# Performance work log

Hardware: AMD Instinct MI355X
Metric: run time of the kernel (lower is better)

Reference implementation:

```python
import jax, jax.numpy as jnp
import numpy as np

K_NEIGHBOURS = 40  # includes self; self is dropped after top-k


def setup_inputs() -> dict:
    key = jax.random.key(0)
    ks = jax.random.split(key, 4)
    B, V, F_in = 4, 4096, 64
    P, S, F_out = 64, 4, 64
    x = jax.random.normal(ks[0], (B, V, F_in), dtype=jnp.float32)
    Wf = jax.random.normal(ks[1], (F_in, P), dtype=jnp.float32) / np.sqrt(F_in)
    bf = jnp.zeros((P,), dtype=jnp.float32)
    Ws = jax.random.normal(ks[2], (F_in, S), dtype=jnp.float32) / np.sqrt(F_in)
    bs = jnp.zeros((S,), dtype=jnp.float32)
    Wo = jax.random.normal(ks[3], (F_in + 2 * P, F_out), dtype=jnp.float32) / np.sqrt(F_in + 2 * P)
    bo = jnpp = jnp.zeros((F_out,), dtype=jnp.float32)
    return {"x": x, "Wf": Wf, "bf": bf, "Ws": Ws, "bs": bs, "Wo": Wo, "bo": bo}


def _euclidean_squared(c):
    # c: [B, V, S] -> [B, V, V] squared pairwise distances
    sq = jnp.sum(c * c, axis=-1)  # [B, V]
    d2 = sq[:, :, None] + sq[:, None, :] - 2.0 * jnp.einsum('bvs,bus->bvu', c, c)
    return d2


def reference(x, Wf, bf, Ws, bs, Wo, bo):
    # learned spatial coordinates and propagated features
    coords = x @ Ws + bs            # [B, V, S]
    feats = x @ Wf + bf             # [B, V, P]

    d2 = _euclidean_squared(coords)                 # [B, V, V]
    neg_vals, idx = jax.lax.top_k(-d2, K_NEIGHBOURS)  # closest first (self at 0)
    nbr_idx = idx[:, :, 1:]                         # [B, V, K-1]
    dist = -neg_vals[:, :, 1:]                      # [B, V, K-1] (>= 0)

    # gauss_of_lin(d * 10) = exp(-|10 d|)
    w = jnp.exp(-jnp.abs(dist * 10.0))              # [B, V, K-1]

    # gather neighbour features per batch: [B, V, K-1, P]
    nf = jax.vmap(lambda f, i: f[i])(feats, nbr_idx)
    nf = nf * w[..., None]

    collected = jnp.concatenate([jnp.max(nf, axis=2), jnp.mean(nf, axis=2)], axis=-1)  # [B, V, 2P]
    updated = jnp.concatenate([x, collected], axis=-1)  # [B, V, F_in + 2P]
    return jnp.tanh(updated @ Wo + bo)
```

## Files before the change

kernel.cpp:

```cpp
#include <hip/hip_runtime.h>
#include <cmath>

#define BB  4
#define VV  4096
#define KK  40
#define FIN 64

typedef float v2f __attribute__((ext_vector_type(2)));

__global__ __launch_bounds__(256) void prep_kernel(
    const float* __restrict__ x, const float* __restrict__ Wf,
    const float* __restrict__ bf, const float* __restrict__ Ws,
    const float* __restrict__ bs,
    float* __restrict__ coords, float* __restrict__ sq,
    float* __restrict__ feats)
{
    int lane = threadIdx.x & 63;
    int wid  = threadIdx.x >> 6;
    int row0 = (blockIdx.x * 4 + wid) * 4;
    const float* xr = x + (size_t)row0 * FIN;

    float a0 = 0.f, a1 = 0.f, a2 = 0.f, a3 = 0.f;
    #pragma unroll 8
    for (int k = 0; k < FIN; ++k) {
        float wf = Wf[k * 64 + lane];
        a0 = fmaf(xr[k],        wf, a0);
        a1 = fmaf(xr[64  + k],  wf, a1);
        a2 = fmaf(xr[128 + k],  wf, a2);
        a3 = fmaf(xr[192 + k],  wf, a3);
    }
    float bfl = bf[lane];
    feats[(size_t)(row0 + 0) * 64 + lane] = a0 + bfl;
    feats[(size_t)(row0 + 1) * 64 + lane] = a1 + bfl;
    feats[(size_t)(row0 + 2) * 64 + lane] = a2 + bfl;
    feats[(size_t)(row0 + 3) * 64 + lane] = a3 + bfl;

    int r  = lane >> 4;
    int s  = (lane >> 2) & 3;
    int kc = lane & 3;
    const float* xrr = x + (size_t)(row0 + r) * FIN + kc * 16;
    const float* wsr = Ws + kc * 16 * 4 + s;
    float c = 0.f;
    #pragma unroll
    for (int k = 0; k < 16; ++k)
        c = fmaf(xrr[k], wsr[k * 4], c);
    c += __shfl_xor(c, 1, 64);
    c += __shfl_xor(c, 2, 64);
    float val = c + bs[s];
    if ((lane & 3) == 0) coords[(size_t)(row0 + r) * 4 + s] = val;
    float p = val * val;
    p += __shfl_xor(p, 4, 64);
    p += __shfl_xor(p, 8, 64);
    if ((lane & 15) == 0) sq[row0 + r] = p;
}

__device__ __forceinline__ unsigned umed3(unsigned a, unsigned b, unsigned c)
{
    unsigned d;
    asm("v_med3_u32 %0, %1, %2, %3" : "=v"(d) : "v"(a), "v"(b), "v"(c));
    return d;
}

__device__ __forceinline__ int cnt_lt4(unsigned m0, unsigned m1,
                                       unsigned m2, unsigned m3,
                                       unsigned cand)
{
    return (int)__popcll(__ballot(m0 < cand))
         + (int)__popcll(__ballot(m1 < cand))
         + (int)__popcll(__ballot(m2 < cand))
         + (int)__popcll(__ballot(m3 < cand));
}

__device__ __forceinline__ unsigned select_thresh(unsigned m0, unsigned m1,
                                                  unsigned m2, unsigned m3)
{
    unsigned M = 0u;
    #pragma unroll
    for (int bit = 30; bit >= 12; --bit) {
        unsigned cand = M | (1u << bit);
        if (cnt_lt4(m0, m1, m2, m3, cand) <= 39) M = cand;
    }
    unsigned Msel = M | 0xFFFu;
    if (cnt_lt4(m0, m1, m2, m3, M + 4096u) != 40) {
        #pragma unroll
        for (int bit = 11; bit >= 0; --bit) {
            unsigned cand = M | (1u << bit);
            if (cnt_lt4(m0, m1, m2, m3, cand) <= 39) M = cand;
        }
        Msel = M;
    }
    return Msel;
}

__device__ __forceinline__ void compact4(unsigned m0, unsigned m1,
                                         unsigned m2, unsigned m3,
                                         unsigned Msel, uint2* dst)
{
    unsigned mn = m0;
    #pragma unroll
    for (int off = 32; off >= 1; off >>= 1) {
        unsigned o = __shfl_xor(mn, off, 64);
        mn = o < mn ? o : mn;
    }
    int base = 0;
    unsigned kk = m0;
    #pragma unroll
    for (int i = 0; i < 4; ++i) {
        bool pred = (kk <= Msel) && (kk != mn);
        unsigned long long mask = __ballot(pred);
        unsigned pos = (unsigned)base +
            __builtin_amdgcn_mbcnt_hi((unsigned)(mask >> 32),
                __builtin_amdgcn_mbcnt_lo((unsigned)mask, 0u));
        if (pred) {
            float d2a = __uint_as_float(kk & 0xFFFFF000u);
            float w   = __expf(-10.f * d2a);
            dst[pos] = make_uint2((kk & 4095u) << 8, __float_as_uint(w));
        }
        base += (int)__popcll(mask);
        kk = (i == 0) ? m1 : (i == 1) ? m2 : m3;
    }
}

__global__ __launch_bounds__(256) void gravnet_kernel(
    const float* __restrict__ x, const float* __restrict__ coords,
    const float* __restrict__ sq, const float* __restrict__ feats,
    const float* __restrict__ Wo, const float* __restrict__ bo,
    float* __restrict__ out)
{
    int lane = threadIdx.x & 63;
    int wid  = threadIdx.x >> 6;
    int q0   = (blockIdx.x * 4 + wid) * 4;
    int b    = q0 >> 12;
    int v0   = q0 & (VV - 1);

    __shared__ uint2               s_nb[4][4][KK];
    __shared__ __align__(16) float s_upd[4][4][192];

    const float4* cb  = (const float4*)(coords + (size_t)b * VV * 4);
    const float*  sqb = sq + (size_t)b * VV;

    float4 cq0 = cb[v0],     cq1 = cb[v0 + 1];
    float4 cq2 = cb[v0 + 2], cq3 = cb[v0 + 3];
    v2f nxA = (v2f){-2.f * cq0.x, -2.f * cq1.x};
    v2f nyA = (v2f){-2.f * cq0.y, -2.f * cq1.y};
    v2f nzA = (v2f){-2.f * cq0.z, -2.f * cq1.z};
    v2f nwA = (v2f){-2.f * cq0.w, -2.f * cq1.w};
    v2f hsA = (v2f){sqb[v0], sqb[v0 + 1]};
    v2f nxB = (v2f){-2.f * cq2.x, -2.f * cq3.x};
    v2f nyB = (v2f){-2.f * cq2.y, -2.f * cq3.y};
    v2f nzB = (v2f){-2.f * cq2.z, -2.f * cq3.z};
    v2f nwB = (v2f){-2.f * cq2.w, -2.f * cq3.w};
    v2f hsB = (v2f){sqb[v0 + 2], sqb[v0 + 3]};

    unsigned k00 = ~0u, k01 = ~0u, k02 = ~0u, k03 = ~0u;
    unsigned k10 = ~0u, k11 = ~0u, k12 = ~0u, k13 = ~0u;
    unsigned k20 = ~0u, k21 = ~0u, k22 = ~0u, k23 = ~0u;
    unsigned k30 = ~0u, k31 = ~0u, k32 = ~0u, k33 = ~0u;

    #pragma unroll 4
    for (int i = 0; i < 64; ++i) {
        int u = i * 64 + lane;
        float4 cu = cb[u];
        float squ = sqb[u];
        v2f accA = hsA + (v2f){squ, squ};
        accA = __builtin_elementwise_fma(nxA, (v2f){cu.x, cu.x}, accA);
        accA = __builtin_elementwise_fma(nyA, (v2f){cu.y, cu.y}, accA);
        accA = __builtin_elementwise_fma(nzA, (v2f){cu.z, cu.z}, accA);
        accA = __builtin_elementwise_fma(nwA, (v2f){cu.w, cu.w}, accA);
        v2f accB = hsB + (v2f){squ, squ};
        accB = __builtin_elementwise_fma(nxB, (v2f){cu.x, cu.x}, accB);
        accB = __builtin_elementwise_fma(nyB, (v2f){cu.y, cu.y}, accB);
        accB = __builtin_elementwise_fma(nzB, (v2f){cu.z, cu.z}, accB);
        accB = __builtin_elementwise_fma(nwB, (v2f){cu.w, cu.w}, accB);

        {
            float d2 = fmaxf(accA.x, 0.f);
            unsigned k = (__float_as_uint(d2) & 0xFFFFF000u) | (unsigned)u;
            unsigned n1 = umed3(k00, k01, k);
            unsigned n2 = umed3(k01, k02, k);
            unsigned n3 = umed3(k02, k03, k);
            k00 = min(k00, k); k01 = n1; k02 = n2; k03 = n3;
        }
        {
            float d2 = fmaxf(accA.y, 0.f);
            unsigned k = (__float_as_uint(d2) & 0xFFFFF000u) | (unsigned)u;
            unsigned n1 = umed3(k10, k11, k);
            unsigned n2 = umed3(k11, k12, k);
            unsigned n3 = umed3(k12, k13, k);
            k10 = min(k10, k); k11 = n1; k12 = n2; k13 = n3;
        }
        {
            float d2 = fmaxf(accB.x, 0.f);
            unsigned k = (__float_as_uint(d2) & 0xFFFFF000u) | (unsigned)u;
            unsigned n1 = umed3(k20, k21, k);
            unsigned n2 = umed3(k21, k22, k);
            unsigned n3 = umed3(k22, k23, k);
            k20 = min(k20, k); k21 = n1; k22 = n2; k23 = n3;
        }
        {
            float d2 = fmaxf(accB.y, 0.f);
            unsigned k = (__float_as_uint(d2) & 0xFFFFF000u) | (unsigned)u;
            unsigned n1 = umed3(k30, k31, k);
            unsigned n2 = umed3(k31, k32, k);
            unsigned n3 = umed3(k32, k33, k);
            k30 = min(k30, k); k31 = n1; k32 = n2; k33 = n3;
        }
    }

    compact4(k00, k01, k02, k03, select_thresh(k00, k01, k02, k03),
             &s_nb[wid][0][0]);
    compact4(k10, k11, k12, k13, select_thresh(k10, k11, k12, k13),
             &s_nb[wid][1][0]);
    compact4(k20, k21, k22, k23, select_thresh(k20, k21, k22, k23),
             &s_nb[wid][2][0]);
    compact4(k30, k31, k32, k33, select_thresh(k30, k31, k32, k33),
             &s_nb[wid][3][0]);

    const float* fb  = feats + (size_t)b * VV * 64;
    const char*  fbl = (const char*)(fb + lane);
    float vmax0 = -INFINITY, vsum0 = 0.f, vmax1 = -INFINITY, vsum1 = 0.f;
    float vmax2 = -INFINITY, vsum2 = 0.f, vmax3 = -INFINITY, vsum3 = 0.f;
    #pragma unroll 3
    for (int j = 0; j < KK - 1; ++j) {
        uint2 n0 = s_nb[wid][0][j];
        uint2 n1 = s_nb[wid][1][j];
        uint2 n2 = s_nb[wid][2][j];
        uint2 n3 = s_nb[wid][3][j];
        float f0 = *(const float*)(fbl + n0.x);
        float f1 = *(const float*)(fbl + n1.x);
        float f2 = *(const float*)(fbl + n2.x);
        float f3 = *(const float*)(fbl + n3.x);
        float v0g = __uint_as_float(n0.y) * f0;
        float v1g = __uint_as_float(n1.y) * f1;
        float v2g = __uint_as_float(n2.y) * f2;
        float v3g = __uint_as_float(n3.y) * f3;
        vmax0 = fmaxf(vmax0, v0g); vsum0 += v0g;
        vmax1 = fmaxf(vmax1, v1g); vsum1 += v1g;
        vmax2 = fmaxf(vmax2, v2g); vsum2 += v2g;
        vmax3 = fmaxf(vmax3, v3g); vsum3 += v3g;
    }

    s_upd[wid][0][lane]       = x[(size_t)(q0 + 0) * 64 + lane];
    s_upd[wid][0][64  + lane] = vmax0;
    s_upd[wid][0][128 + lane] = vsum0 * (1.0f / 39.0f);
    s_upd[wid][1][lane]       = x[(size_t)(q0 + 1) * 64 + lane];
    s_upd[wid][1][64  + lane] = vmax1;
    s_upd[wid][1][128 + lane] = vsum1 * (1.0f / 39.0f);
    s_upd[wid][2][lane]       = x[(size_t)(q0 + 2) * 64 + lane];
    s_upd[wid][2][64  + lane] = vmax2;
    s_upd[wid][2][128 + lane] = vsum2 * (1.0f / 39.0f);
    s_upd[wid][3][lane]       = x[(size_t)(q0 + 3) * 64 + lane];
    s_upd[wid][3][64  + lane] = vmax3;
    s_upd[wid][3][128 + lane] = vsum3 * (1.0f / 39.0f);

    float bol = bo[lane];
    float acc0 = bol, acc1 = bol, acc2 = bol, acc3 = bol;
    #pragma unroll 4
    for (int j4 = 0; j4 < 48; ++j4) {
        float wo0 = Wo[(j4 * 4 + 0) * 64 + lane];
        float wo1 = Wo[(j4 * 4 + 1) * 64 + lane];
        float wo2 = Wo[(j4 * 4 + 2) * 64 + lane];
        float wo3 = Wo[(j4 * 4 + 3) * 64 + lane];
        float4 u0 = *(const float4*)&s_upd[wid][0][j4 * 4];
        float4 u1 = *(const float4*)&s_upd[wid][1][j4 * 4];
        float4 u2 = *(const float4*)&s_upd[wid][2][j4 * 4];
        float4 u3 = *(const float4*)&s_upd[wid][3][j4 * 4];
        acc0 = fmaf(u0.x, wo0, acc0);  acc1 = fmaf(u1.x, wo0, acc1);
        acc2 = fmaf(u2.x, wo0, acc2);  acc3 = fmaf(u3.x, wo0, acc3);
        acc0 = fmaf(u0.y, wo1, acc0);  acc1 = fmaf(u1.y, wo1, acc1);
        acc2 = fmaf(u2.y, wo1, acc2);  acc3 = fmaf(u3.y, wo1, acc3);
        acc0 = fmaf(u0.z, wo2, acc0);  acc1 = fmaf(u1.z, wo2, acc1);
        acc2 = fmaf(u2.z, wo2, acc2);  acc3 = fmaf(u3.z, wo2, acc3);
        acc0 = fmaf(u0.w, wo3, acc0);  acc1 = fmaf(u1.w, wo3, acc1);
        acc2 = fmaf(u2.w, wo3, acc2);  acc3 = fmaf(u3.w, wo3, acc3);
    }
    float e0 = __expf(2.f * acc0);
    float e1 = __expf(2.f * acc1);
    float e2 = __expf(2.f * acc2);
    float e3 = __expf(2.f * acc3);
    out[(size_t)(q0 + 0) * 64 + lane] = 1.f - __fdividef(2.f, e0 + 1.f);
    out[(size_t)(q0 + 1) * 64 + lane] = 1.f - __fdividef(2.f, e1 + 1.f);
    out[(size_t)(q0 + 2) * 64 + lane] = 1.f - __fdividef(2.f, e2 + 1.f);
    out[(size_t)(q0 + 3) * 64 + lane] = 1.f - __fdividef(2.f, e3 + 1.f);
}

extern "C" void kernel_launch(void* const* d_in, const int* in_sizes, int n_in,
                              void* d_out, int out_size, void* d_ws, size_t ws_size,
                              hipStream_t stream)
{
    (void)in_sizes; (void)n_in; (void)out_size; (void)ws_size;
    const float* x  = (const float*)d_in[0];
    const float* Wf = (const float*)d_in[1];
    const float* bf = (const float*)d_in[2];
    const float* Ws = (const float*)d_in[3];
    const float* bs = (const float*)d_in[4];
    const float* Wo = (const float*)d_in[5];
    const float* bo = (const float*)d_in[6];
    float* out = (float*)d_out;

    float* coords = (float*)d_ws;
    float* sq     = coords + (size_t)BB * VV * 4;
    float* feats  = sq + (size_t)BB * VV;

    prep_kernel<<<BB * VV / 16, 256, 0, stream>>>(x, Wf, bf, Ws, bs,
                                                  coords, sq, feats);
    gravnet_kernel<<<BB * VV / 16, 256, 0, stream>>>(x, coords, sq, feats,
                                                     Wo, bo, out);
}
```

Before: 127.0 us.

## Split candidate scan across wave pairs and merge per-lane top-4 via LDS

Each query group of 4 is now handled by two waves, each scanning half of the candidate points. The per-lane sorted top-4 lists are exchanged through shared memory and merged with a bitonic-style min step, then each wave compacts, gathers and projects 2 of the 4 queries. This doubles the grid and halves the serial scan per wave to increase parallelism, at the cost of block-wide barriers, LDS traffic and duplicated Wo loads.

```diff
diff --git a/kernel.cpp b/kernel.cpp
--- a/kernel.cpp
+++ b/kernel.cpp
@@ -128,13 +128,17 @@
     float* __restrict__ out)
 {
     int lane = threadIdx.x & 63;
-    int wid  = threadIdx.x >> 6;
-    int q0   = (blockIdx.x * 4 + wid) * 4;
-    int b    = q0 >> 12;
-    int v0   = q0 & (VV - 1);
-
-    __shared__ uint2               s_nb[4][4][KK];
-    __shared__ __align__(16) float s_upd[4][4][192];
+    int w    = threadIdx.x >> 6;
+    int quad = w >> 1;
+    int half = w & 1;
+    int qb   = blockIdx.x * 8 + quad * 4;
+    int b    = (blockIdx.x * 8) >> 12;
+    int v0   = qb & (VV - 1);
+
+    __shared__ __align__(16) char smem[16384];
+    uint4* s_mrg = (uint4*)smem;
+    uint2* s_nb  = (uint2*)smem;
+    float* s_upd = (float*)(smem + 8 * KK * 8);
 
     const float4* cb  = (const float4*)(coords + (size_t)b * VV * 4);
     const float*  sqb = sq + (size_t)b * VV;
@@ -157,8 +161,9 @@
     unsigned k20 = ~0u, k21 = ~0u, k22 = ~0u, k23 = ~0u;
     unsigned k30 = ~0u, k31 = ~0u, k32 = ~0u, k33 = ~0u;
 
+    int i0 = half * 32;
     #pragma unroll 4
-    for (int i = 0; i < 64; ++i) {
+    for (int i = i0; i < i0 + 32; ++i) {
         int u = i * 64 + lane;
         float4 cu = cb[u];
         float squ = sqb[u];
@@ -207,81 +212,75 @@
         }
     }
 
-    compact4(k00, k01, k02, k03, select_thresh(k00, k01, k02, k03),
-             &s_nb[wid][0][0]);
-    compact4(k10, k11, k12, k13, select_thresh(k10, k11, k12, k13),
-             &s_nb[wid][1][0]);
-    compact4(k20, k21, k22, k23, select_thresh(k20, k21, k22, k23),
-             &s_nb[wid][2][0]);
-    compact4(k30, k31, k32, k33, select_thresh(k30, k31, k32, k33),
-             &s_nb[wid][3][0]);
+    s_mrg[(w * 4 + 0) * 64 + lane] = make_uint4(k00, k01, k02, k03);
+    s_mrg[(w * 4 + 1) * 64 + lane] = make_uint4(k10, k11, k12, k13);
+    s_mrg[(w * 4 + 2) * 64 + lane] = make_uint4(k20, k21, k22, k23);
+    s_mrg[(w * 4 + 3) * 64 + lane] = make_uint4(k30, k31, k32, k33);
+    __syncthreads();
+
+    int p   = w ^ 1;
+    int lq0 = half * 2;
+    uint4 pb0 = s_mrg[(p * 4 + lq0)     * 64 + lane];
+    uint4 pb1 = s_mrg[(p * 4 + lq0 + 1) * 64 + lane];
+    unsigned oa0 = half ? k20 : k00, oa1 = half ? k21 : k01;
+    unsigned oa2 = half ? k22 : k02, oa3 = half ? k23 : k03;
+    unsigned ob0 = half ? k30 : k10, ob1 = half ? k31 : k11;
+    unsigned ob2 = half ? k32 : k12, ob3 = half ? k33 : k13;
+    __syncthreads();
+
+    unsigned d0 = min(oa0, pb0.w), d1 = min(oa1, pb0.z);
+    unsigned d2 = min(oa2, pb0.y), d3 = min(oa3, pb0.x);
+    unsigned A0 = min(d0, d3), A3 = max(d0, d3);
+    unsigned e0 = min(ob0, pb1.w), e1 = min(ob1, pb1.z);
+    unsigned e2 = min(ob2, pb1.y), e3 = min(ob3, pb1.x);
+    unsigned B0 = min(e0, e3), B3 = max(e0, e3);
+
+    int s0 = w * 2, s1 = w * 2 + 1;
+    compact4(A0, d1, d2, A3, select_thresh(A0, d1, d2, A3), &s_nb[s0 * KK]);
+    compact4(B0, e1, e2, B3, select_thresh(B0, e1, e2, B3), &s_nb[s1 * KK]);
 
     const float* fb  = feats + (size_t)b * VV * 64;
     const char*  fbl = (const char*)(fb + lane);
     float vmax0 = -INFINITY, vsum0 = 0.f, vmax1 = -INFINITY, vsum1 = 0.f;
-    float vmax2 = -INFINITY, vsum2 = 0.f, vmax3 = -INFINITY, vsum3 = 0.f;
-    #pragma unroll 3
+    #pragma unroll 6
     for (int j = 0; j < KK - 1; ++j) {
-        uint2 n0 = s_nb[wid][0][j];
-        uint2 n1 = s_nb[wid][1][j];
-        uint2 n2 = s_nb[wid][2][j];
-        uint2 n3 = s_nb[wid][3][j];
+        uint2 n0 = s_nb[s0 * KK + j];
+        uint2 n1 = s_nb[s1 * KK + j];
         float f0 = *(const float*)(fbl + n0.x);
         float f1 = *(const float*)(fbl + n1.x);
-        float f2 = *(const float*)(fbl + n2.x);
-        float f3 = *(const float*)(fbl + n3.x);
-        float v0g = __uint_as_float(n0.y) * f0;
-        float v1g = __uint_as_float(n1.y) * f1;
-        float v2g = __uint_as_float(n2.y) * f2;
-        float v3g = __uint_as_float(n3.y) * f3;
-        vmax0 = fmaxf(vmax0, v0g); vsum0 += v0g;
-        vmax1 = fmaxf(vmax1, v1g); vsum1 += v1g;
-        vmax2 = fmaxf(vmax2, v2g); vsum2 += v2g;
-        vmax3 = fmaxf(vmax3, v3g); vsum3 += v3g;
-    }
-
-    s_upd[wid][0][lane]       = x[(size_t)(q0 + 0) * 64 + lane];
-    s_upd[wid][0][64  + lane] = vmax0;
-    s_upd[wid][0][128 + lane] = vsum0 * (1.0f / 39.0f);
-    s_upd[wid][1][lane]       = x[(size_t)(q0 + 1) * 64 + lane];
-    s_upd[wid][1][64  + lane] = vmax1;
-    s_upd[wid][1][128 + lane] = vsum1 * (1.0f / 39.0f);
-    s_upd[wid][2][lane]       = x[(size_t)(q0 + 2) * 64 + lane];
-    s_upd[wid][2][64  + lane] = vmax2;
-    s_upd[wid][2][128 + lane] = vsum2 * (1.0f / 39.0f);
-    s_upd[wid][3][lane]       = x[(size_t)(q0 + 3) * 64 + lane];
-    s_upd[wid][3][64  + lane] = vmax3;
-    s_upd[wid][3][128 + lane] = vsum3 * (1.0f / 39.0f);
+        float g0 = __uint_as_float(n0.y) * f0;
+        float g1 = __uint_as_float(n1.y) * f1;
+        vmax0 = fmaxf(vmax0, g0); vsum0 += g0;
+        vmax1 = fmaxf(vmax1, g1); vsum1 += g1;
+    }
+
+    int q0g = qb + lq0, q1g = qb + lq0 + 1;
+    s_upd[s0 * 192 + lane]       = x[(size_t)q0g * 64 + lane];
+    s_upd[s0 * 192 + 64  + lane] = vmax0;
+    s_upd[s0 * 192 + 128 + lane] = vsum0 * (1.0f / 39.0f);
+    s_upd[s1 * 192 + lane]       = x[(size_t)q1g * 64 + lane];
+    s_upd[s1 * 192 + 64  + lane] = vmax1;
+    s_upd[s1 * 192 + 128 + lane] = vsum1 * (1.0f / 39.0f);
 
     float bol = bo[lane];
-    float acc0 = bol, acc1 = bol, acc2 = bol, acc3 = bol;
+    float acc0 = bol, acc1 = bol;
     #pragma unroll 4
     for (int j4 = 0; j4 < 48; ++j4) {
         float wo0 = Wo[(j4 * 4 + 0) * 64 + lane];
         float wo1 = Wo[(j4 * 4 + 1) * 64 + lane];
         float wo2 = Wo[(j4 * 4 + 2) * 64 + lane];
         float wo3 = Wo[(j4 * 4 + 3) * 64 + lane];
-        float4 u0 = *(const float4*)&s_upd[wid][0][j4 * 4];
-        float4 u1 = *(const float4*)&s_upd[wid][1][j4 * 4];
-        float4 u2 = *(const float4*)&s_upd[wid][2][j4 * 4];
-        float4 u3 = *(const float4*)&s_upd[wid][3][j4 * 4];
+        float4 u0 = *(const float4*)&s_upd[s0 * 192 + j4 * 4];
+        float4 u1 = *(const float4*)&s_upd[s1 * 192 + j4 * 4];
         acc0 = fmaf(u0.x, wo0, acc0);  acc1 = fmaf(u1.x, wo0, acc1);
-        acc2 = fmaf(u2.x, wo0, acc2);  acc3 = fmaf(u3.x, wo0, acc3);
         acc0 = fmaf(u0.y, wo1, acc0);  acc1 = fmaf(u1.y, wo1, acc1);
-        acc2 = fmaf(u2.y, wo1, acc2);  acc3 = fmaf(u3.y, wo1, acc3);
         acc0 = fmaf(u0.z, wo2, acc0);  acc1 = fmaf(u1.z, wo2, acc1);
-        acc2 = fmaf(u2.z, wo2, acc2);  acc3 = fmaf(u3.z, wo2, acc3);
         acc0 = fmaf(u0.w, wo3, acc0);  acc1 = fmaf(u1.w, wo3, acc1);
-        acc2 = fmaf(u2.w, wo3, acc2);  acc3 = fmaf(u3.w, wo3, acc3);
-    }
-    float e0 = __expf(2.f * acc0);
-    float e1 = __expf(2.f * acc1);
-    float e2 = __expf(2.f * acc2);
-    float e3 = __expf(2.f * acc3);
-    out[(size_t)(q0 + 0) * 64 + lane] = 1.f - __fdividef(2.f, e0 + 1.f);
-    out[(size_t)(q0 + 1) * 64 + lane] = 1.f - __fdividef(2.f, e1 + 1.f);
-    out[(size_t)(q0 + 2) * 64 + lane] = 1.f - __fdividef(2.f, e2 + 1.f);
-    out[(size_t)(q0 + 3) * 64 + lane] = 1.f - __fdividef(2.f, e3 + 1.f);
+    }
+    float e0t = __expf(2.f * acc0);
+    float e1t = __expf(2.f * acc1);
+    out[(size_t)q0g * 64 + lane] = 1.f - __fdividef(2.f, e0t + 1.f);
+    out[(size_t)q1g * 64 + lane] = 1.f - __fdividef(2.f, e1t + 1.f);
 }
 
 extern "C" void kernel_launch(void* const* d_in, const int* in_sizes, int n_in,
@@ -304,6 +303,6 @@
 
     prep_kernel<<<BB * VV / 16, 256, 0, stream>>>(x, Wf, bf, Ws, bs,
                                                   coords, sq, feats);
-    gravnet_kernel<<<BB * VV / 16, 256, 0, stream>>>(x, coords, sq, feats,
-                                                     Wo, bo, out);
-}
+    gravnet_kernel<<<BB * VV / 8, 256, 0, stream>>>(x, coords, sq, feats,
+                                                    Wo, bo, out);
+}
```

Result: faster. 124.0 us (-2.3%).
